# Kernel optimization log

Hardware: AMD Instinct MI355X
Metric: run time of the kernel (lower is better)

## Reference

```python
import jax, jax.numpy as jnp
import numpy as np

H = 4096
W = 4096
N_BOXES = 200000


def gaussian_mount() -> jnp.ndarray:
    # 3x3 gaussian, sigma=1, normalized so max == 1 (matches gaussian_2d + /max)
    y, x = np.ogrid[-1:2, -1:2]
    g = np.exp(-(x * x + y * y) / 2.0)
    g[g < np.finfo(g.dtype).eps * g.max()] = 0
    g = g / g.max()
    return jnp.asarray(g, dtype=jnp.float32)


def setup_inputs() -> dict:
    key = jax.random.key(0)
    boxes = jax.random.uniform(key, (N_BOXES, 4), dtype=jnp.float32)  # cx,cy,w,h in [0,1)
    return {"boxes": boxes, "mount": gaussian_mount(), "w": W, "h": H}


def reference(boxes, mount, w, h):
    # centers in pixel coords (floor via int cast, same as .long())
    cx = (boxes[:, 0] * w).astype(jnp.int32)  # [B]
    cy = (boxes[:, 1] * h).astype(jnp.int32)  # [B]

    sizemap = jnp.zeros((2, h, w), dtype=jnp.float32).at[:, cy, cx].set(boxes[:, 2:4].T)

    # A 3x3 mount is stamped only when the full window fits inside the image
    # (the torch loop's slice produces a too-small target otherwise and skips).
    valid = (cx >= 1) & (cx <= w - 2) & (cy >= 1) & (cy <= h - 2)  # [B]

    off = jnp.arange(-1, 2)
    rows = jnp.clip(cy, 1, h - 2)[:, None, None] + off[:, None]  # [B,3,3] (clip keeps idx in-range)
    cols = jnp.clip(cx, 1, w - 2)[:, None, None] + off[None, :]  # [B,3,3]
    vals = jnp.where(valid[:, None, None], mount[None, :, :], 0.0)  # invalid -> 0, max no-op

    # order-independent scatter-max (sequential torch.max loop is equivalent)
    heat = jnp.zeros((h, w), dtype=jnp.float32).at[rows, cols].max(vals)

    heatmap = heat[None, None]      # [1,1,h,w]
    sizemap = sizemap[None]         # [1,2,h,w]
    return heatmap, sizemap
```

## Files before the change

### kernel.cpp

```cpp
#include <hip/hip_runtime.h>

#define IMG_H 4096
#define IMG_W 4096
#define NPIX (IMG_H * IMG_W)

#define TILE 64
#define TILES_X (IMG_W / TILE)
#define TILES_Y (IMG_H / TILE)
#define NBINS (TILES_X * TILES_Y)
#define BIN_CAP 256
#define CSTRIDE 32

__global__ __launch_bounds__(256) void bin_boxes_kernel(
    const float* __restrict__ boxes,
    int* __restrict__ counts,
    int* __restrict__ bins,
    int nboxes)
{
    int b = blockIdx.x * blockDim.x + threadIdx.x;
    if (b >= nboxes) return;
    float4 bx = reinterpret_cast<const float4*>(boxes)[b];
    int cx = (int)(bx.x * (float)IMG_W);
    int cy = (int)(bx.y * (float)IMG_H);
    int valid = (cx >= 1 && cx <= IMG_W - 2 && cy >= 1 && cy <= IMG_H - 2) ? 1 : 0;
    int pack = b | ((cx & 63) << 18) | ((cy & 63) << 24) | (valid << 30);
    int bin = (cy >> 6) * TILES_X + (cx >> 6);
    int slot = atomicAdd(&counts[bin * CSTRIDE], 1);
    if (slot < BIN_CAP) bins[bin * BIN_CAP + slot] = pack;
}

__global__ __launch_bounds__(256) void tile_kernel(
    const float* __restrict__ boxes,
    const float* __restrict__ mount,
    const int* __restrict__ counts,
    const int* __restrict__ bins,
    float* __restrict__ heat,
    float* __restrict__ s0,
    float* __restrict__ s1)
{
    __shared__ __align__(16) int lidx[TILE * TILE];
    __shared__ __align__(16) unsigned int bm[TILE + 2][4];
    __shared__ int pfx[10];
    __shared__ int bbase[9];

    int tid = threadIdx.x;
    int tile = blockIdx.x;
    int tx = tile & (TILES_X - 1);
    int ty = tile >> 6;

    if (tid < 16) {
        int cnt = 0, base = 0;
        int nty = ty + tid / 3 - 1;
        int ntx = tx + (tid % 3) - 1;
        if (tid < 9 && (unsigned)nty < (unsigned)TILES_Y && (unsigned)ntx < (unsigned)TILES_X) {
            int bin = nty * TILES_X + ntx;
            cnt = min(counts[bin * CSTRIDE], BIN_CAP);
            base = bin * BIN_CAP;
        }
        int inc = cnt;
#pragma unroll
        for (int d = 1; d < 16; d <<= 1) {
            int v = __shfl_up(inc, d, 16);
            if (tid >= d) inc += v;
        }
        if (tid < 10) pfx[tid] = inc - cnt;
        if (tid < 9) bbase[tid] = base;
    }

    int4 neg1 = make_int4(-1, -1, -1, -1);
#pragma unroll
    for (int i = 0; i < 4; ++i)
        reinterpret_cast<int4*>(lidx)[tid + 256 * i] = neg1;
    if (tid < TILE + 2)
        *reinterpret_cast<uint4*>(&bm[tid][0]) = make_uint4(0u, 0u, 0u, 0u);
    __syncthreads();

    int S = pfx[9];
    for (int i = tid; i < S; i += 256) {
        int j = 0;
        while (pfx[j + 1] <= i) ++j;
        int p = bins[bbase[j] + (i - pfx[j])];
        int lx = (p >> 18) & 63;
        int ly = (p >> 24) & 63;
        if (j == 4) atomicMax(&lidx[ly * TILE + lx], p);
        if (p & (1 << 30)) {
            int Lx = lx + (j % 3) * 64 - 64;
            int Ly = ly + (j / 3) * 64 - 64;
            if (Lx >= -1 && Lx <= TILE && Ly >= -1 && Ly <= TILE) {
                int pos = Lx + 1;
                atomicOr(&bm[Ly + 1][pos >> 5], 1u << (pos & 31));
            }
        }
    }
    __syncthreads();

    float mvC = mount[4];
    float mvE = mount[1];
    float mvK = mount[0];
    int ty0 = ty * TILE, tx0 = tx * TILE;

#pragma unroll
    for (int pass = 0; pass < 4; ++pass) {
        int idx = pass * 1024 + tid * 4;
        int r = idx >> 6;
        int xb = idx & 63;

        uint4 w0 = *(const uint4*)&bm[r][0];
        uint4 w1 = *(const uint4*)&bm[r + 1][0];
        uint4 w2 = *(const uint4*)&bm[r + 2][0];
        unsigned long long V0 = ((unsigned long long)w0.y << 32) | w0.x;
        unsigned long long V1 = ((unsigned long long)w1.y << 32) | w1.x;
        unsigned long long V2 = ((unsigned long long)w2.y << 32) | w2.x;
        if (xb) {
            V0 = (V0 >> xb) | ((unsigned long long)w0.z << (64 - xb));
            V1 = (V1 >> xb) | ((unsigned long long)w1.z << (64 - xb));
            V2 = (V2 >> xb) | ((unsigned long long)w2.z << (64 - xb));
        }
        unsigned int C = (unsigned int)(V1 >> 1);
        unsigned int E = (unsigned int)V1 | (unsigned int)(V1 >> 2)
                       | (unsigned int)(V0 >> 1) | (unsigned int)(V2 >> 1);
        unsigned int K = (unsigned int)V0 | (unsigned int)(V0 >> 2)
                       | (unsigned int)V2 | (unsigned int)(V2 >> 2);

        float h[4];
#pragma unroll
        for (int jj = 0; jj < 4; ++jj) {
            float v = 0.f;
            if ((K >> jj) & 1) v = mvK;
            if ((E >> jj) & 1) v = mvE;
            if ((C >> jj) & 1) v = mvC;
            h[jj] = v;
        }

        int g = (ty0 + r) * IMG_W + tx0 + xb;
        *reinterpret_cast<float4*>(&heat[g]) = make_float4(h[0], h[1], h[2], h[3]);

        int4 iv = *reinterpret_cast<const int4*>(&lidx[idx]);
        float4 ow = make_float4(0.f, 0.f, 0.f, 0.f);
        float4 oh = make_float4(0.f, 0.f, 0.f, 0.f);
        if (iv.x >= 0) { float4 bb = reinterpret_cast<const float4*>(boxes)[iv.x & 0x3FFFF]; ow.x = bb.z; oh.x = bb.w; }
        if (iv.y >= 0) { float4 bb = reinterpret_cast<const float4*>(boxes)[iv.y & 0x3FFFF]; ow.y = bb.z; oh.y = bb.w; }
        if (iv.z >= 0) { float4 bb = reinterpret_cast<const float4*>(boxes)[iv.z & 0x3FFFF]; ow.z = bb.z; oh.z = bb.w; }
        if (iv.w >= 0) { float4 bb = reinterpret_cast<const float4*>(boxes)[iv.w & 0x3FFFF]; ow.w = bb.z; oh.w = bb.w; }
        *reinterpret_cast<float4*>(&s0[g]) = ow;
        *reinterpret_cast<float4*>(&s1[g]) = oh;
    }
}

extern "C" void kernel_launch(void* const* d_in, const int* in_sizes, int n_in,
                              void* d_out, int out_size, void* d_ws, size_t ws_size,
                              hipStream_t stream) {
    const float* boxes = (const float*)d_in[0];
    const float* mount = (const float*)d_in[1];
    int nboxes = in_sizes[0] / 4;

    float* out  = (float*)d_out;
    float* heat = out;
    float* s0   = out + NPIX;
    float* s1   = out + 2 * NPIX;

    int* counts = (int*)d_ws;
    int* bins   = counts + NBINS * CSTRIDE;

    hipMemsetAsync(counts, 0, NBINS * CSTRIDE * sizeof(int), stream);

    int bgrid = (nboxes + 255) / 256;
    bin_boxes_kernel<<<bgrid, 256, 0, stream>>>(boxes, counts, bins, nboxes);

    tile_kernel<<<NBINS, 256, 0, stream>>>(boxes, mount, counts, bins, heat, s0, s1);
}
```

Before: 214.0 us.

## Build per-tile center bitmaps in global memory during binning, drop neighbor bin scans

```diff
diff --git a/kernel.cpp b/kernel.cpp
--- a/kernel.cpp
+++ b/kernel.cpp
@@ -11,22 +11,45 @@
 #define BIN_CAP 256
 #define CSTRIDE 32
 
-__global__ __launch_bounds__(256) void bin_boxes_kernel(
+#define BMW 4
+#define BMROWS (TILE + 2)
+#define BM_WORDS (BMROWS * BMW)
+
+__global__ __launch_bounds__(256) void bin_stamp_kernel(
     const float* __restrict__ boxes,
     int* __restrict__ counts,
     int* __restrict__ bins,
+    unsigned int* __restrict__ gbm,
     int nboxes)
 {
-    int b = blockIdx.x * blockDim.x + threadIdx.x;
+    int b = blockIdx.x * 256 + threadIdx.x;
     if (b >= nboxes) return;
     float4 bx = reinterpret_cast<const float4*>(boxes)[b];
     int cx = (int)(bx.x * (float)IMG_W);
     int cy = (int)(bx.y * (float)IMG_H);
+    int lx = cx & 63, ly = cy & 63;
+    int tx = cx >> 6, ty = cy >> 6;
     int valid = (cx >= 1 && cx <= IMG_W - 2 && cy >= 1 && cy <= IMG_H - 2) ? 1 : 0;
-    int pack = b | ((cx & 63) << 18) | ((cy & 63) << 24) | (valid << 30);
-    int bin = (cy >> 6) * TILES_X + (cx >> 6);
+
+    int pack = b | (lx << 18) | (ly << 24) | (valid << 30);
+    int bin = ty * TILES_X + tx;
     int slot = atomicAdd(&counts[bin * CSTRIDE], 1);
     if (slot < BIN_CAP) bins[bin * BIN_CAP + slot] = pack;
+
+    if (valid) {
+        int dxlo = (lx == 0  && tx > 0)           ? -1 : 0;
+        int dxhi = (lx == 63 && tx < TILES_X - 1) ?  1 : 0;
+        int dylo = (ly == 0  && ty > 0)           ? -1 : 0;
+        int dyhi = (ly == 63 && ty < TILES_Y - 1) ?  1 : 0;
+        for (int dy = dylo; dy <= dyhi; ++dy)
+            for (int dx = dxlo; dx <= dxhi; ++dx) {
+                int t   = (ty + dy) * TILES_X + (tx + dx);
+                int row = ly - 64 * dy + 1;
+                int pos = lx - 64 * dx + 1;
+                atomicOr(&gbm[t * BM_WORDS + row * BMW + (pos >> 5)],
+                         1u << (pos & 31));
+            }
+    }
 }
 
 __global__ __launch_bounds__(256) void tile_kernel(
@@ -34,69 +57,42 @@
     const float* __restrict__ mount,
     const int* __restrict__ counts,
     const int* __restrict__ bins,
+    const unsigned int* __restrict__ gbm,
     float* __restrict__ heat,
     float* __restrict__ s0,
     float* __restrict__ s1)
 {
     __shared__ __align__(16) int lidx[TILE * TILE];
-    __shared__ __align__(16) unsigned int bm[TILE + 2][4];
-    __shared__ int pfx[10];
-    __shared__ int bbase[9];
+    __shared__ __align__(16) unsigned int bm[BMROWS][BMW];
 
     int tid = threadIdx.x;
     int tile = blockIdx.x;
     int tx = tile & (TILES_X - 1);
     int ty = tile >> 6;
 
-    if (tid < 16) {
-        int cnt = 0, base = 0;
-        int nty = ty + tid / 3 - 1;
-        int ntx = tx + (tid % 3) - 1;
-        if (tid < 9 && (unsigned)nty < (unsigned)TILES_Y && (unsigned)ntx < (unsigned)TILES_X) {
-            int bin = nty * TILES_X + ntx;
-            cnt = min(counts[bin * CSTRIDE], BIN_CAP);
-            base = bin * BIN_CAP;
-        }
-        int inc = cnt;
-#pragma unroll
-        for (int d = 1; d < 16; d <<= 1) {
-            int v = __shfl_up(inc, d, 16);
-            if (tid >= d) inc += v;
-        }
-        if (tid < 10) pfx[tid] = inc - cnt;
-        if (tid < 9) bbase[tid] = base;
-    }
+    float mvC = mount[4];
+    float mvE = mount[1];
+    float mvK = mount[0];
+    int cnt = min(counts[tile * CSTRIDE], BIN_CAP);
+
+    if (tid < BMROWS)
+        reinterpret_cast<uint4*>(bm)[tid] =
+            reinterpret_cast<const uint4*>(gbm + (size_t)tile * BM_WORDS)[tid];
 
     int4 neg1 = make_int4(-1, -1, -1, -1);
 #pragma unroll
     for (int i = 0; i < 4; ++i)
         reinterpret_cast<int4*>(lidx)[tid + 256 * i] = neg1;
-    if (tid < TILE + 2)
-        *reinterpret_cast<uint4*>(&bm[tid][0]) = make_uint4(0u, 0u, 0u, 0u);
     __syncthreads();
 
-    int S = pfx[9];
-    for (int i = tid; i < S; i += 256) {
-        int j = 0;
-        while (pfx[j + 1] <= i) ++j;
-        int p = bins[bbase[j] + (i - pfx[j])];
+    for (int i = tid; i < cnt; i += 256) {
+        int p = bins[tile * BIN_CAP + i];
         int lx = (p >> 18) & 63;
         int ly = (p >> 24) & 63;
-        if (j == 4) atomicMax(&lidx[ly * TILE + lx], p);
-        if (p & (1 << 30)) {
-            int Lx = lx + (j % 3) * 64 - 64;
-            int Ly = ly + (j / 3) * 64 - 64;
-            if (Lx >= -1 && Lx <= TILE && Ly >= -1 && Ly <= TILE) {
-                int pos = Lx + 1;
-                atomicOr(&bm[Ly + 1][pos >> 5], 1u << (pos & 31));
-            }
-        }
+        atomicMax(&lidx[ly * TILE + lx], p);
     }
     __syncthreads();
 
-    float mvC = mount[4];
-    float mvE = mount[1];
-    float mvK = mount[0];
     int ty0 = ty * TILE, tx0 = tx * TILE;
 
 #pragma unroll
@@ -159,13 +155,17 @@
     float* s0   = out + NPIX;
     float* s1   = out + 2 * NPIX;
 
-    int* counts = (int*)d_ws;
-    int* bins   = counts + NBINS * CSTRIDE;
+    int* counts       = (int*)d_ws;
+    unsigned int* gbm = (unsigned int*)(counts + NBINS * CSTRIDE);
+    int* bins         = (int*)(gbm + (size_t)NBINS * BM_WORDS);
 
-    hipMemsetAsync(counts, 0, NBINS * CSTRIDE * sizeof(int), stream);
+    hipMemsetAsync(counts, 0,
+                   NBINS * CSTRIDE * sizeof(int) +
+                   (size_t)NBINS * BM_WORDS * sizeof(unsigned int), stream);
 
     int bgrid = (nboxes + 255) / 256;
-    bin_boxes_kernel<<<bgrid, 256, 0, stream>>>(boxes, counts, bins, nboxes);
+    bin_stamp_kernel<<<bgrid, 256, 0, stream>>>(boxes, counts, bins, gbm, nboxes);
 
-    tile_kernel<<<NBINS, 256, 0, stream>>>(boxes, mount, counts, bins, heat, s0, s1);
+    tile_kernel<<<NBINS, 256, 0, stream>>>(boxes, mount, counts, bins, gbm,
+                                           heat, s0, s1);
 }
```

After: 221.1 us. +3.3%, slower.

## Fuse zeroing, binning and tile stages into one cooperative persistent kernel

Applied to the files above, without the earlier changes.

```diff
diff --git a/kernel.cpp b/kernel.cpp
--- a/kernel.cpp
+++ b/kernel.cpp
@@ -1,4 +1,7 @@
 #include <hip/hip_runtime.h>
+#include <hip/hip_cooperative_groups.h>
+
+namespace cg = cooperative_groups;
 
 #define IMG_H 4096
 #define IMG_W 4096
@@ -11,139 +14,147 @@
 #define BIN_CAP 256
 #define CSTRIDE 32
 
-__global__ __launch_bounds__(256) void bin_boxes_kernel(
+__global__ __launch_bounds__(256, 8) void fused_kernel(
     const float* __restrict__ boxes,
+    const float* __restrict__ mount,
     int* __restrict__ counts,
     int* __restrict__ bins,
-    int nboxes)
-{
-    int b = blockIdx.x * blockDim.x + threadIdx.x;
-    if (b >= nboxes) return;
-    float4 bx = reinterpret_cast<const float4*>(boxes)[b];
-    int cx = (int)(bx.x * (float)IMG_W);
-    int cy = (int)(bx.y * (float)IMG_H);
-    int valid = (cx >= 1 && cx <= IMG_W - 2 && cy >= 1 && cy <= IMG_H - 2) ? 1 : 0;
-    int pack = b | ((cx & 63) << 18) | ((cy & 63) << 24) | (valid << 30);
-    int bin = (cy >> 6) * TILES_X + (cx >> 6);
-    int slot = atomicAdd(&counts[bin * CSTRIDE], 1);
-    if (slot < BIN_CAP) bins[bin * BIN_CAP + slot] = pack;
-}
-
-__global__ __launch_bounds__(256) void tile_kernel(
-    const float* __restrict__ boxes,
-    const float* __restrict__ mount,
-    const int* __restrict__ counts,
-    const int* __restrict__ bins,
     float* __restrict__ heat,
     float* __restrict__ s0,
-    float* __restrict__ s1)
+    float* __restrict__ s1,
+    int nboxes)
 {
     __shared__ __align__(16) int lidx[TILE * TILE];
     __shared__ __align__(16) unsigned int bm[TILE + 2][4];
     __shared__ int pfx[10];
     __shared__ int bbase[9];
 
+    cg::grid_group grid = cg::this_grid();
     int tid = threadIdx.x;
-    int tile = blockIdx.x;
-    int tx = tile & (TILES_X - 1);
-    int ty = tile >> 6;
+    int bid = blockIdx.x;
+    int nb  = gridDim.x;
+    int gthreads = nb * 256;
 
-    if (tid < 16) {
-        int cnt = 0, base = 0;
-        int nty = ty + tid / 3 - 1;
-        int ntx = tx + (tid % 3) - 1;
-        if (tid < 9 && (unsigned)nty < (unsigned)TILES_Y && (unsigned)ntx < (unsigned)TILES_X) {
-            int bin = nty * TILES_X + ntx;
-            cnt = min(counts[bin * CSTRIDE], BIN_CAP);
-            base = bin * BIN_CAP;
-        }
-        int inc = cnt;
-#pragma unroll
-        for (int d = 1; d < 16; d <<= 1) {
-            int v = __shfl_up(inc, d, 16);
-            if (tid >= d) inc += v;
-        }
-        if (tid < 10) pfx[tid] = inc - cnt;
-        if (tid < 9) bbase[tid] = base;
+    for (int i = bid * 256 + tid; i < NBINS; i += gthreads)
+        counts[i * CSTRIDE] = 0;
+    grid.sync();
+
+    for (int b = bid * 256 + tid; b < nboxes; b += gthreads) {
+        float4 bx = reinterpret_cast<const float4*>(boxes)[b];
+        int cx = (int)(bx.x * (float)IMG_W);
+        int cy = (int)(bx.y * (float)IMG_H);
+        int valid = (cx >= 1 && cx <= IMG_W - 2 && cy >= 1 && cy <= IMG_H - 2) ? 1 : 0;
+        int pack = b | ((cx & 63) << 18) | ((cy & 63) << 24) | (valid << 30);
+        int bin = (cy >> 6) * TILES_X + (cx >> 6);
+        int slot = atomicAdd(&counts[bin * CSTRIDE], 1);
+        if (slot < BIN_CAP) bins[bin * BIN_CAP + slot] = pack;
     }
-
-    int4 neg1 = make_int4(-1, -1, -1, -1);
-#pragma unroll
-    for (int i = 0; i < 4; ++i)
-        reinterpret_cast<int4*>(lidx)[tid + 256 * i] = neg1;
-    if (tid < TILE + 2)
-        *reinterpret_cast<uint4*>(&bm[tid][0]) = make_uint4(0u, 0u, 0u, 0u);
-    __syncthreads();
-
-    int S = pfx[9];
-    for (int i = tid; i < S; i += 256) {
-        int j = 0;
-        while (pfx[j + 1] <= i) ++j;
-        int p = bins[bbase[j] + (i - pfx[j])];
-        int lx = (p >> 18) & 63;
-        int ly = (p >> 24) & 63;
-        if (j == 4) atomicMax(&lidx[ly * TILE + lx], p);
-        if (p & (1 << 30)) {
-            int Lx = lx + (j % 3) * 64 - 64;
-            int Ly = ly + (j / 3) * 64 - 64;
-            if (Lx >= -1 && Lx <= TILE && Ly >= -1 && Ly <= TILE) {
-                int pos = Lx + 1;
-                atomicOr(&bm[Ly + 1][pos >> 5], 1u << (pos & 31));
-            }
-        }
-    }
-    __syncthreads();
+    grid.sync();
 
     float mvC = mount[4];
     float mvE = mount[1];
     float mvK = mount[0];
-    int ty0 = ty * TILE, tx0 = tx * TILE;
+
+    for (int tile = bid; tile < NBINS; tile += nb) {
+        int tx = tile & (TILES_X - 1);
+        int ty = tile >> 6;
+
+        __syncthreads();
+
+        if (tid < 16) {
+            int cnt = 0, base = 0;
+            int nty = ty + tid / 3 - 1;
+            int ntx = tx + (tid % 3) - 1;
+            if (tid < 9 && (unsigned)nty < (unsigned)TILES_Y && (unsigned)ntx < (unsigned)TILES_X) {
+                int bin = nty * TILES_X + ntx;
+                cnt = min(counts[bin * CSTRIDE], BIN_CAP);
+                base = bin * BIN_CAP;
+            }
+            int inc = cnt;
+#pragma unroll
+            for (int d = 1; d < 16; d <<= 1) {
+                int v = __shfl_up(inc, d, 16);
+                if (tid >= d) inc += v;
+            }
+            if (tid < 10) pfx[tid] = inc - cnt;
+            if (tid < 9) bbase[tid] = base;
+        }
+
+        int4 neg1 = make_int4(-1, -1, -1, -1);
+#pragma unroll
+        for (int i = 0; i < 4; ++i)
+            reinterpret_cast<int4*>(lidx)[tid + 256 * i] = neg1;
+        if (tid < TILE + 2)
+            *reinterpret_cast<uint4*>(&bm[tid][0]) = make_uint4(0u, 0u, 0u, 0u);
+        __syncthreads();
+
+        int S = pfx[9];
+        for (int i = tid; i < S; i += 256) {
+            int j = 0;
+            while (pfx[j + 1] <= i) ++j;
+            int p = bins[bbase[j] + (i - pfx[j])];
+            int lx = (p >> 18) & 63;
+            int ly = (p >> 24) & 63;
+            if (j == 4) atomicMax(&lidx[ly * TILE + lx], p);
+            if (p & (1 << 30)) {
+                int Lx = lx + (j % 3) * 64 - 64;
+                int Ly = ly + (j / 3) * 64 - 64;
+                if (Lx >= -1 && Lx <= TILE && Ly >= -1 && Ly <= TILE) {
+                    int pos = Lx + 1;
+                    atomicOr(&bm[Ly + 1][pos >> 5], 1u << (pos & 31));
+                }
+            }
+        }
+        __syncthreads();
+
+        int ty0 = ty * TILE, tx0 = tx * TILE;
 
 #pragma unroll
-    for (int pass = 0; pass < 4; ++pass) {
-        int idx = pass * 1024 + tid * 4;
-        int r = idx >> 6;
-        int xb = idx & 63;
+        for (int pass = 0; pass < 4; ++pass) {
+            int idx = pass * 1024 + tid * 4;
+            int r = idx >> 6;
+            int xb = idx & 63;
 
-        uint4 w0 = *(const uint4*)&bm[r][0];
-        uint4 w1 = *(const uint4*)&bm[r + 1][0];
-        uint4 w2 = *(const uint4*)&bm[r + 2][0];
-        unsigned long long V0 = ((unsigned long long)w0.y << 32) | w0.x;
-        unsigned long long V1 = ((unsigned long long)w1.y << 32) | w1.x;
-        unsigned long long V2 = ((unsigned long long)w2.y << 32) | w2.x;
-        if (xb) {
-            V0 = (V0 >> xb) | ((unsigned long long)w0.z << (64 - xb));
-            V1 = (V1 >> xb) | ((unsigned long long)w1.z << (64 - xb));
-            V2 = (V2 >> xb) | ((unsigned long long)w2.z << (64 - xb));
+            uint4 w0 = *(const uint4*)&bm[r][0];
+            uint4 w1 = *(const uint4*)&bm[r + 1][0];
+            uint4 w2 = *(const uint4*)&bm[r + 2][0];
+            unsigned long long V0 = ((unsigned long long)w0.y << 32) | w0.x;
+            unsigned long long V1 = ((unsigned long long)w1.y << 32) | w1.x;
+            unsigned long long V2 = ((unsigned long long)w2.y << 32) | w2.x;
+            if (xb) {
+                V0 = (V0 >> xb) | ((unsigned long long)w0.z << (64 - xb));
+                V1 = (V1 >> xb) | ((unsigned long long)w1.z << (64 - xb));
+                V2 = (V2 >> xb) | ((unsigned long long)w2.z << (64 - xb));
+            }
+            unsigned int C = (unsigned int)(V1 >> 1);
+            unsigned int E = (unsigned int)V1 | (unsigned int)(V1 >> 2)
+                           | (unsigned int)(V0 >> 1) | (unsigned int)(V2 >> 1);
+            unsigned int K = (unsigned int)V0 | (unsigned int)(V0 >> 2)
+                           | (unsigned int)V2 | (unsigned int)(V2 >> 2);
+
+            float h[4];
+#pragma unroll
+            for (int jj = 0; jj < 4; ++jj) {
+                float v = 0.f;
+                if ((K >> jj) & 1) v = mvK;
+                if ((E >> jj) & 1) v = mvE;
+                if ((C >> jj) & 1) v = mvC;
+                h[jj] = v;
+            }
+
+            int g = (ty0 + r) * IMG_W + tx0 + xb;
+            *reinterpret_cast<float4*>(&heat[g]) = make_float4(h[0], h[1], h[2], h[3]);
+
+            int4 iv = *reinterpret_cast<const int4*>(&lidx[idx]);
+            float4 ow = make_float4(0.f, 0.f, 0.f, 0.f);
+            float4 oh = make_float4(0.f, 0.f, 0.f, 0.f);
+            if (iv.x >= 0) { float4 bb = reinterpret_cast<const float4*>(boxes)[iv.x & 0x3FFFF]; ow.x = bb.z; oh.x = bb.w; }
+            if (iv.y >= 0) { float4 bb = reinterpret_cast<const float4*>(boxes)[iv.y & 0x3FFFF]; ow.y = bb.z; oh.y = bb.w; }
+            if (iv.z >= 0) { float4 bb = reinterpret_cast<const float4*>(boxes)[iv.z & 0x3FFFF]; ow.z = bb.z; oh.z = bb.w; }
+            if (iv.w >= 0) { float4 bb = reinterpret_cast<const float4*>(boxes)[iv.w & 0x3FFFF]; ow.w = bb.z; oh.w = bb.w; }
+            *reinterpret_cast<float4*>(&s0[g]) = ow;
+            *reinterpret_cast<float4*>(&s1[g]) = oh;
         }
-        unsigned int C = (unsigned int)(V1 >> 1);
-        unsigned int E = (unsigned int)V1 | (unsigned int)(V1 >> 2)
-                       | (unsigned int)(V0 >> 1) | (unsigned int)(V2 >> 1);
-        unsigned int K = (unsigned int)V0 | (unsigned int)(V0 >> 2)
-                       | (unsigned int)V2 | (unsigned int)(V2 >> 2);
-
-        float h[4];
-#pragma unroll
-        for (int jj = 0; jj < 4; ++jj) {
-            float v = 0.f;
-            if ((K >> jj) & 1) v = mvK;
-            if ((E >> jj) & 1) v = mvE;
-            if ((C >> jj) & 1) v = mvC;
-            h[jj] = v;
-        }
-
-        int g = (ty0 + r) * IMG_W + tx0 + xb;
-        *reinterpret_cast<float4*>(&heat[g]) = make_float4(h[0], h[1], h[2], h[3]);
-
-        int4 iv = *reinterpret_cast<const int4*>(&lidx[idx]);
-        float4 ow = make_float4(0.f, 0.f, 0.f, 0.f);
-        float4 oh = make_float4(0.f, 0.f, 0.f, 0.f);
-        if (iv.x >= 0) { float4 bb = reinterpret_cast<const float4*>(boxes)[iv.x & 0x3FFFF]; ow.x = bb.z; oh.x = bb.w; }
-        if (iv.y >= 0) { float4 bb = reinterpret_cast<const float4*>(boxes)[iv.y & 0x3FFFF]; ow.y = bb.z; oh.y = bb.w; }
-        if (iv.z >= 0) { float4 bb = reinterpret_cast<const float4*>(boxes)[iv.z & 0x3FFFF]; ow.z = bb.z; oh.z = bb.w; }
-        if (iv.w >= 0) { float4 bb = reinterpret_cast<const float4*>(boxes)[iv.w & 0x3FFFF]; ow.w = bb.z; oh.w = bb.w; }
-        *reinterpret_cast<float4*>(&s0[g]) = ow;
-        *reinterpret_cast<float4*>(&s1[g]) = oh;
     }
 }
 
@@ -162,10 +173,17 @@
     int* counts = (int*)d_ws;
     int* bins   = counts + NBINS * CSTRIDE;
 
-    hipMemsetAsync(counts, 0, NBINS * CSTRIDE * sizeof(int), stream);
+    static int bpc = 0;
+    if (bpc == 0) {
+        hipError_t e = hipOccupancyMaxActiveBlocksPerMultiprocessor(
+            &bpc, fused_kernel, 256, 0);
+        if (e != hipSuccess || bpc < 1) bpc = 4;
+    }
+    int nblocks = bpc * 256;
+    if (nblocks > NBINS) nblocks = NBINS;
 
-    int bgrid = (nboxes + 255) / 256;
-    bin_boxes_kernel<<<bgrid, 256, 0, stream>>>(boxes, counts, bins, nboxes);
-
-    tile_kernel<<<NBINS, 256, 0, stream>>>(boxes, mount, counts, bins, heat, s0, s1);
+    void* args[] = { (void*)&boxes, (void*)&mount, (void*)&counts, (void*)&bins,
+                     (void*)&heat, (void*)&s0, (void*)&s1, (void*)&nboxes };
+    hipLaunchCooperativeKernel((void*)fused_kernel, dim3(nblocks), dim3(256),
+                               args, 0, stream);
 }
```

Result: slower. 392.1 us (+83.2%).
